# Kernel tuning notes

Measured on AMD Instinct MI355X. Metric: run time of the kernel, lower is better.

Reference implementation:

```python
import jax, jax.numpy as jnp
import numpy as np

N = 50000
E = 800000
NUM_GRAPHS = 128
X_IN, HID, EDGE_DIM = 64, 64, 16


def setup_inputs() -> dict:
    key = jax.random.key(0)
    ks = jax.random.split(key, 9)
    s = 0.05
    inp = {
        'x': jax.random.normal(ks[0], (N, X_IN), jnp.float32),
        'edge_index': jax.random.randint(ks[1], (2, E), 0, N, dtype=jnp.int32),
        'edge_attr': jax.random.normal(ks[2], (E, EDGE_DIM), jnp.float32),
        'batch': jnp.sort(jax.random.randint(ks[3], (N,), 0, NUM_GRAPHS, dtype=jnp.int32)),
        'w_fc1': jax.random.normal(ks[4], (EDGE_DIM, 1), jnp.float32) * s,
        'b_fc1': jnp.zeros((1,), jnp.float32),
    }
    dims = [(X_IN, HID), (HID, HID * 2), (HID * 2, HID)]
    for i, (din, dout) in enumerate(dims):
        k1, k2, k3 = jax.random.split(ks[5 + i], 3)
        inp[f'w1_{i}'] = jax.random.normal(k1, (din, dout), jnp.float32) * s
        inp[f'b1_{i}'] = jnp.zeros((dout,), jnp.float32)
        inp[f'w2_{i}'] = jax.random.normal(k2, (din, dout), jnp.float32) * s
        inp[f'w3_{i}'] = jax.random.normal(k3, (din, dout), jnp.float32) * s
        inp[f'b3_{i}'] = jnp.zeros((dout,), jnp.float32)
    return inp


def leconv(x, src, dst, ew, w1, b1, w2, w3, b3):
    # PyG LEConv: out_i = lin3(x_i) + sum_{j->i} e_ji * (lin1(x_j) - lin2(x_i))
    a = x @ w1 + b1          # lin1 (bias=True)   [N, out]
    b = x @ w2               # lin2 (bias=False)  [N, out]
    msg = ew[:, None] * (a[src] - b[dst])          # [E, out]
    agg = jax.ops.segment_sum(msg, dst, num_segments=N)
    return agg + x @ w3 + b3  # lin3 (bias=True)


def reference(x, edge_index, edge_attr, batch,
              w_fc1, b_fc1,
              w1_0, b1_0, w2_0, w3_0, b3_0,
              w1_1, b1_1, w2_1, w3_1, b3_1,
              w1_2, b1_2, w2_2, w3_2, b3_2):
    src, dst = edge_index[0], edge_index[1]
    ew = (edge_attr @ w_fc1 + b_fc1)[:, 0]         # fc1(edge_attr).squeeze(-1) -> [E]
    h = jax.nn.elu(leconv(x, src, dst, ew, w1_0, b1_0, w2_0, w3_0, b3_0))
    h = jax.nn.elu(leconv(h, src, dst, ew, w1_1, b1_1, w2_1, w3_1, b3_1))
    h = jax.nn.elu(leconv(h, src, dst, ew, w1_2, b1_2, w2_2, w3_2, b3_2))
    # global max pool over nodes of each graph -> [NUM_GRAPHS, HID]
    return jax.ops.segment_max(h, batch, num_segments=NUM_GRAPHS)
```

## Files before the change

### kernel.cpp

```cpp
#include <hip/hip_runtime.h>
#include <math.h>

#define N_NODES 50000
#define N_EDGES 800000
#define NUM_GRAPHS_ 128
#define SCAN_NB 98
#define NPASS 4
#define NODES_PER_PASS 12500
#define HCHUNKS 128
#define EDGES_PER_CHUNK 6250
#define HWORDS 12500
#define TS_BPH 196

typedef unsigned short u16;
typedef unsigned int u32;
typedef __attribute__((ext_vector_type(8))) short bf16x8;
typedef __attribute__((ext_vector_type(4))) float f32x4;

__device__ __forceinline__ float elu_f(float v) {
    return v > 0.f ? v : (__expf(v) - 1.f);
}
__device__ __forceinline__ u16 f2bf(float f) {
    u32 u = __float_as_uint(f);
    u += 0x7FFFu + ((u >> 16) & 1u);
    return (u16)(u >> 16);
}
__device__ __forceinline__ float bf2f(u16 h) {
    return __uint_as_float(((u32)h) << 16);
}
__device__ __forceinline__ void bfpair(u32 v, float& lo, float& hi) {
    lo = __uint_as_float(v << 16);
    hi = __uint_as_float(v & 0xFFFF0000u);
}
__device__ __forceinline__ u32 packbf(float lo, float hi) {
    return (u32)f2bf(lo) | ((u32)f2bf(hi) << 16);
}

__global__ void prep_kernel(const float* __restrict__ edge_attr,
                            const float* __restrict__ w_fc1,
                            const float* __restrict__ b_fc1,
                            const int* __restrict__ edge_index,
                            float* __restrict__ ew,
                            u16* __restrict__ dst16,
                            const float* __restrict__ x, u16* __restrict__ xb,
                            const float* __restrict__ w3_0, const float* __restrict__ w1_0, const float* __restrict__ w2_0,
                            const float* __restrict__ w3_1, const float* __restrict__ w1_1, const float* __restrict__ w2_1,
                            const float* __restrict__ w3_2, const float* __restrict__ w1_2, const float* __restrict__ w2_2,
                            u16* __restrict__ bp0, u16* __restrict__ bp1, u16* __restrict__ bp2) {
    const int b = blockIdx.x;
    if (b < 3125) {
        const int e = b * 256 + threadIdx.x;
        const float4* ea = (const float4*)(edge_attr + (size_t)e * 16);
        const float4* wf = (const float4*)w_fc1;
        float acc = b_fc1[0];
#pragma unroll
        for (int i = 0; i < 4; i++) {
            float4 a = ea[i], w = wf[i];
            acc += a.x * w.x + a.y * w.y + a.z * w.z + a.w * w.w;
        }
        ew[e] = acc;
        dst16[e] = (u16)edge_index[N_EDGES + e];
    } else if (b < 6250) {
        const int g = (b - 3125) * 256 + threadIdx.x;
        float4 v = ((const float4*)x)[g];
        uint2 o;
        o.x = packbf(v.x, v.y);
        o.y = packbf(v.z, v.w);
        ((uint2*)xb)[g] = o;
    } else {
        const int t = (b - 6250) * 256 + threadIdx.x;
        u16 buf[8];
        if (t < 4608) {
            int DOUT, lid;
            const float *w3, *w1, *w2;
            u16* bp;
            if (t < 1536) { DOUT = 64;  lid = t;        w3 = w3_0; w1 = w1_0; w2 = w2_0; bp = bp0; }
            else          { DOUT = 128; lid = t - 1536; w3 = w3_1; w1 = w1_1; w2 = w2_1; bp = bp1; }
            const int NT = DOUT / 16;
            const int lane = lid & 63;
            const int fragid = lid >> 6;
            const int chunk = fragid / NT;
            const int ntile = fragid % NT;
            const int n = ntile * 16 + (lane & 15);
            const int kbase = chunk * 32 + (lane >> 4) * 8;
#pragma unroll
            for (int j = 0; j < 8; j++) {
                int k = kbase + j;
                int region = k / 64;
                int kk = k - region * 64;
                float v = (region == 0) ? w3[kk * DOUT + n]
                        : (region == 1) ? w1[kk * DOUT + n]
                                        : -w2[kk * DOUT + n];
                buf[j] = f2bf(v);
            }
            *(bf16x8*)(bp + ((size_t)lid << 3)) = *(bf16x8*)buf;
        } else if (t < 7680) {
            const int lid = t - 4608;
            const int NT = 12;
            const int lane = lid & 63;
            const int fragid = lid >> 6;
            const int chunk = fragid / NT;
            const int ntile = fragid % NT;
            const int n = ntile * 16 + (lane & 15);
            const int kbase = chunk * 32 + (lane >> 4) * 8;
#pragma unroll
            for (int j = 0; j < 8; j++) {
                int k = kbase + j;
                float v = (n < 64)  ? w3_2[k * 64 + n]
                        : (n < 128) ? -w2_2[k * 64 + (n - 64)]
                                    : w1_2[k * 64 + (n - 128)];
                buf[j] = f2bf(v);
            }
            *(bf16x8*)(bp2 + ((size_t)lid << 3)) = *(bf16x8*)buf;
        }
    }
}

__global__ __launch_bounds__(256) void deg_hist_kernel(const u16* __restrict__ dst16,
                                                       u32* __restrict__ partial) {
    __shared__ u32 bins[HWORDS];
    const int c = blockIdx.x >> 1;
    const int p = blockIdx.x & 1;
    const int t = threadIdx.x;
    for (int i = t; i < HWORDS; i += 256) bins[i] = 0;
    __syncthreads();
    const int base = c * EDGES_PER_CHUNK;
    const int nlo = p * 25000;
    for (int i = t; i < EDGES_PER_CHUNK; i += 256) {
        const int b = (int)dst16[base + i] - nlo;
        if ((unsigned)b < 25000u)
            atomicAdd(&bins[b >> 1], 1u << ((b & 1) * 16));
    }
    __syncthreads();
    u32* outp = partial + (size_t)blockIdx.x * HWORDS;
    for (int i = t; i < HWORDS; i += 256) outp[i] = bins[i];
}

__global__ __launch_bounds__(256) void scan_chunks_kernel(const u32* __restrict__ partial,
                                                          u32* __restrict__ prefpack,
                                                          u32* __restrict__ degpack) {
    __shared__ u32 qsums[4][64];
    const int t = threadIdx.x;
    const int p = (blockIdx.x >= TS_BPH) ? 1 : 0;
    const int wh0 = (blockIdx.x - p * TS_BPH) << 6;
    const int wl = t & 63;
    const int cq = t >> 6;
    const int wh = wh0 + wl;
    const bool ok = wh < HWORDS;

    u32 vals[32];
#pragma unroll
    for (int i = 0; i < 32; i++) {
        const int c = cq * 32 + i;
        vals[i] = ok ? partial[(size_t)((c << 1) + p) * HWORDS + wh] : 0u;
    }
    u32 s = 0;
#pragma unroll
    for (int i = 0; i < 32; i++) s += vals[i];
    qsums[cq][wl] = s;
    __syncthreads();
    u32 run = 0;
#pragma unroll
    for (int j = 0; j < 4; j++)
        if (j < cq) run += qsums[j][wl];

    if (ok) {
        const int g = p * HWORDS + wh;
#pragma unroll
        for (int i = 0; i < 32; i++) {
            const int c = cq * 32 + i;
            prefpack[(size_t)c * 25000 + g] = run;
            run += vals[i];
        }
        if (cq == 3) degpack[g] = run;
    }
}

__global__ __launch_bounds__(256) void scan1_kernel(const u32* __restrict__ degpack,
                                                    int* __restrict__ rowptr,
                                                    int* __restrict__ blk_sums) {
    __shared__ int sh[256];
    const int t = threadIdx.x;
    const int base = blockIdx.x * 512;
    const int i0 = base + 2 * t, i1 = i0 + 1;
    int d0 = 0, d1 = 0;
    if (i0 < N_NODES) {
        u32 v = degpack[i0 >> 1];
        d0 = (int)(v & 0xFFFFu);
        d1 = (int)(v >> 16);
    }
    const int pair = d0 + d1;
    int v = pair;
    sh[t] = v;
    __syncthreads();
#pragma unroll
    for (int off = 1; off < 256; off <<= 1) {
        int add = (t >= off) ? sh[t - off] : 0;
        __syncthreads();
        v += add;
        sh[t] = v;
        __syncthreads();
    }
    const int excl = v - pair;
    if (i0 < N_NODES) rowptr[i0] = excl;
    if (i1 < N_NODES) rowptr[i1] = excl + d0;
    if (t == 255) blk_sums[blockIdx.x] = v;
}

__global__ __launch_bounds__(128) void scan2_kernel(const int* __restrict__ blk_sums,
                                                    int* __restrict__ blk_offs,
                                                    int* __restrict__ rowptr) {
    __shared__ int sh[128];
    const int t = threadIdx.x;
    const int orig = (t < SCAN_NB) ? blk_sums[t] : 0;
    int v = orig;
    sh[t] = v;
    __syncthreads();
#pragma unroll
    for (int off = 1; off < 128; off <<= 1) {
        int add = (t >= off) ? sh[t - off] : 0;
        __syncthreads();
        v += add;
        sh[t] = v;
        __syncthreads();
    }
    if (t < SCAN_NB) blk_offs[t] = v - orig;
    if (t == 127) rowptr[N_NODES] = v;
}

__global__ void scan3_kernel(int* __restrict__ rowptr,
                             const int* __restrict__ blk_offs) {
    int i = blockIdx.x * blockDim.x + threadIdx.x;
    if (i >= N_NODES) return;
    rowptr[i] += blk_offs[i >> 9];
}

__global__ __launch_bounds__(256) void place_kernel(const int* __restrict__ edge_index,
                                                    const float* __restrict__ ew,
                                                    const u16* __restrict__ dst16,
                                                    const int* __restrict__ rowptr,
                                                    const u32* __restrict__ prefpack,
                                                    int2* __restrict__ csr) {
    __shared__ int lcur[NODES_PER_PASS];
    const int pass = blockIdx.x & (NPASS - 1);
    const int c = blockIdx.x >> 2;
    const int lo = pass * NODES_PER_PASS;
    const int t = threadIdx.x;
    for (int i = t; i < NODES_PER_PASS; i += 256) lcur[i] = 0;
    __syncthreads();
    const int base = c * EDGES_PER_CHUNK;
    for (int i = t; i < EDGES_PER_CHUNK; i += 256) {
        const int e = base + i;
        const int d = (int)dst16[e];
        const int dl = d - lo;
        if ((unsigned)dl < (unsigned)NODES_PER_PASS) {
            u32 pw = prefpack[(size_t)c * 25000 + (d >> 1)];
            int pref = (int)((pw >> ((d & 1) * 16)) & 0xFFFFu);
            int lpos = atomicAdd(&lcur[dl], 1);
            int2 ent;
            ent.x = edge_index[e];
            ent.y = __float_as_int(ew[e]);
            csr[rowptr[d] + pref + lpos] = ent;
        }
    }
}

__global__ __launch_bounds__(1024) void fused_l0(
    const u16* __restrict__ xb, const int* __restrict__ rowptr,
    const int2* __restrict__ csr, const u16* __restrict__ Bp0,
    const float* __restrict__ bias1, const float* __restrict__ bias3,
    float* __restrict__ cvec, u16* __restrict__ h1out) {
    __shared__ u16 A[64][200];
    __shared__ float csh[64];
    const int tid = threadIdx.x;
    const int wv = tid >> 6;
    const int lane = tid & 63;
    const int node_base = blockIdx.x * 64;
    const uint2* x2 = (const uint2*)xb;
    const int cg = lane & 15;
    const int eg = lane >> 4;

    for (int k = 0; k < 4; k++) {
        const int row = wv * 4 + k;
        const int node = node_base + row;
        float a0 = 0.f, a1 = 0.f, a2 = 0.f, a3 = 0.f;
        float b0 = 0.f, b1 = 0.f, b2 = 0.f, b3 = 0.f;
        float wsum = 0.f;
        if (node < N_NODES) {
            const int beg = rowptr[node];
            const int end = rowptr[node + 1];
            int p = beg + eg;
            for (; p + 4 < end; p += 8) {
                int2 e0 = csr[p];
                int2 e1 = csr[p + 4];
                float w0 = __int_as_float(e0.y);
                float w1 = __int_as_float(e1.y);
                uint2 v0 = x2[(size_t)e0.x * 16 + cg];
                uint2 v1 = x2[(size_t)e1.x * 16 + cg];
                float f0, f1, f2, f3, g0, g1, g2, g3;
                bfpair(v0.x, f0, f1); bfpair(v0.y, f2, f3);
                bfpair(v1.x, g0, g1); bfpair(v1.y, g2, g3);
                a0 += w0 * f0; a1 += w0 * f1; a2 += w0 * f2; a3 += w0 * f3;
                b0 += w1 * g0; b1 += w1 * g1; b2 += w1 * g2; b3 += w1 * g3;
                wsum += w0 + w1;
            }
            if (p < end) {
                int2 e0 = csr[p];
                float w0 = __int_as_float(e0.y);
                uint2 v0 = x2[(size_t)e0.x * 16 + cg];
                float f0, f1, f2, f3;
                bfpair(v0.x, f0, f1); bfpair(v0.y, f2, f3);
                a0 += w0 * f0; a1 += w0 * f1; a2 += w0 * f2; a3 += w0 * f3;
                wsum += w0;
            }
        }
        a0 += b0; a1 += b1; a2 += b2; a3 += b3;
#pragma unroll
        for (int off = 32; off >= 16; off >>= 1) {
            a0 += __shfl_xor(a0, off);
            a1 += __shfl_xor(a1, off);
            a2 += __shfl_xor(a2, off);
            a3 += __shfl_xor(a3, off);
            wsum += __shfl_xor(wsum, off);
        }
        if (lane < 16) {
            const float cn = wsum;
            uint2 hv = (node < N_NODES) ? x2[(size_t)node * 16 + cg] : (uint2){0u, 0u};
            uint2 so;
            so.x = packbf(a0, a1);
            so.y = packbf(a2, a3);
            *(uint2*)&A[row][cg * 4] = hv;
            *(uint2*)&A[row][64 + cg * 4] = so;
            float h0, h1f, h2f, h3f;
            bfpair(hv.x, h0, h1f); bfpair(hv.y, h2f, h3f);
            uint2 co;
            co.x = packbf(cn * h0, cn * h1f);
            co.y = packbf(cn * h2f, cn * h3f);
            *(uint2*)&A[row][128 + cg * 4] = co;
            if (cg == 0) {
                csh[row] = cn;
                if (node < N_NODES) cvec[node] = cn;
            }
        }
    }
    __syncthreads();

    const int l15 = lane & 15;
    const int q = lane >> 4;
    const int qo = q * 8;
    const int mt = wv >> 2, nt = wv & 3;
    f32x4 acc = {0.f, 0.f, 0.f, 0.f};
#pragma unroll
    for (int chunk = 0; chunk < 6; chunk++) {
        bf16x8 a = *(const bf16x8*)&A[mt * 16 + l15][chunk * 32 + qo];
        bf16x8 b = *(const bf16x8*)(Bp0 + (((size_t)(chunk * 4 + nt) * 64 + lane) << 3));
        acc = __builtin_amdgcn_mfma_f32_16x16x32_bf16(a, b, acc, 0, 0, 0);
    }
    const int col = nt * 16 + l15;
    const float B3 = bias3[col];
    const float B1 = bias1[col];
#pragma unroll
    for (int reg = 0; reg < 4; reg++) {
        const int lrow = mt * 16 + q * 4 + reg;
        const int row = node_base + lrow;
        if (row < N_NODES) {
            const float val = acc[reg] + B3 + csh[lrow] * B1;
            h1out[(size_t)row * 64 + col] = f2bf(elu_f(val));
        }
    }
}

__global__ __launch_bounds__(1024) void fused_l1(
    const u16* __restrict__ h1in, const int* __restrict__ rowptr,
    const int2* __restrict__ csr, const u16* __restrict__ Bp1,
    const u16* __restrict__ Bp2, const float* __restrict__ bias1,
    const float* __restrict__ bias3, u16* __restrict__ zuy) {
    __shared__ u16 A[64][200];
    __shared__ u16 ht[64][136];
    __shared__ float csh[64];
    const int tid = threadIdx.x;
    const int wv = tid >> 6;
    const int lane = tid & 63;
    const int node_base = blockIdx.x * 64;
    const uint2* x2 = (const uint2*)h1in;
    const int cg = lane & 15;
    const int eg = lane >> 4;

    for (int k = 0; k < 4; k++) {
        const int row = wv * 4 + k;
        const int node = node_base + row;
        float a0 = 0.f, a1 = 0.f, a2 = 0.f, a3 = 0.f;
        float b0 = 0.f, b1 = 0.f, b2 = 0.f, b3 = 0.f;
        float wsum = 0.f;
        if (node < N_NODES) {
            const int beg = rowptr[node];
            const int end = rowptr[node + 1];
            int p = beg + eg;
            for (; p + 4 < end; p += 8) {
                int2 e0 = csr[p];
                int2 e1 = csr[p + 4];
                float w0 = __int_as_float(e0.y);
                float w1 = __int_as_float(e1.y);
                uint2 v0 = x2[(size_t)e0.x * 16 + cg];
                uint2 v1 = x2[(size_t)e1.x * 16 + cg];
                float f0, f1, f2, f3, g0, g1, g2, g3;
                bfpair(v0.x, f0, f1); bfpair(v0.y, f2, f3);
                bfpair(v1.x, g0, g1); bfpair(v1.y, g2, g3);
                a0 += w0 * f0; a1 += w0 * f1; a2 += w0 * f2; a3 += w0 * f3;
                b0 += w1 * g0; b1 += w1 * g1; b2 += w1 * g2; b3 += w1 * g3;
                wsum += w0 + w1;
            }
            if (p < end) {
                int2 e0 = csr[p];
                float w0 = __int_as_float(e0.y);
                uint2 v0 = x2[(size_t)e0.x * 16 + cg];
                float f0, f1, f2, f3;
                bfpair(v0.x, f0, f1); bfpair(v0.y, f2, f3);
                a0 += w0 * f0; a1 += w0 * f1; a2 += w0 * f2; a3 += w0 * f3;
                wsum += w0;
            }
        }
        a0 += b0; a1 += b1; a2 += b2; a3 += b3;
#pragma unroll
        for (int off = 32; off >= 16; off >>= 1) {
            a0 += __shfl_xor(a0, off);
            a1 += __shfl_xor(a1, off);
            a2 += __shfl_xor(a2, off);
            a3 += __shfl_xor(a3, off);
            wsum += __shfl_xor(wsum, off);
        }
        if (lane < 16) {
            const float cn = wsum;
            uint2 hv = (node < N_NODES) ? x2[(size_t)node * 16 + cg] : (uint2){0u, 0u};
            uint2 so;
            so.x = packbf(a0, a1);
            so.y = packbf(a2, a3);
            *(uint2*)&A[row][cg * 4] = hv;
            *(uint2*)&A[row][64 + cg * 4] = so;
            float h0, h1f, h2f, h3f;
            bfpair(hv.x, h0, h1f); bfpair(hv.y, h2f, h3f);
            uint2 co;
            co.x = packbf(cn * h0, cn * h1f);
            co.y = packbf(cn * h2f, cn * h3f);
            *(uint2*)&A[row][128 + cg * 4] = co;
            if (cg == 0) csh[row] = cn;
        }
    }
    __syncthreads();

    const int l15 = lane & 15;
    const int q = lane >> 4;
    const int qo = q * 8;

    {
        const int mt = wv >> 2;
        const int nt0 = (wv & 3) * 2;
        f32x4 acc0 = {0.f, 0.f, 0.f, 0.f};
        f32x4 acc1 = {0.f, 0.f, 0.f, 0.f};
#pragma unroll
        for (int chunk = 0; chunk < 6; chunk++) {
            bf16x8 a = *(const bf16x8*)&A[mt * 16 + l15][chunk * 32 + qo];
            bf16x8 bf0 = *(const bf16x8*)(Bp1 + (((size_t)(chunk * 8 + nt0) * 64 + lane) << 3));
            bf16x8 bf1 = *(const bf16x8*)(Bp1 + (((size_t)(chunk * 8 + nt0 + 1) * 64 + lane) << 3));
            acc0 = __builtin_amdgcn_mfma_f32_16x16x32_bf16(a, bf0, acc0, 0, 0, 0);
            acc1 = __builtin_amdgcn_mfma_f32_16x16x32_bf16(a, bf1, acc1, 0, 0, 0);
        }
#pragma unroll
        for (int ni = 0; ni < 2; ni++) {
            const int col = (nt0 + ni) * 16 + l15;
            const float B3 = bias3[col];
            const float B1 = bias1[col];
            const f32x4 av = ni ? acc1 : acc0;
#pragma unroll
            for (int reg = 0; reg < 4; reg++) {
                const int lrow = mt * 16 + q * 4 + reg;
                ht[lrow][col] = f2bf(elu_f(av[reg] + B3 + csh[lrow] * B1));
            }
        }
    }
    __syncthreads();

    {
        const int mt = wv >> 2;
        const int ntb = (wv & 3) * 3;
        f32x4 acc[3] = {};
#pragma unroll
        for (int chunk = 0; chunk < 4; chunk++) {
            bf16x8 a = *(const bf16x8*)&ht[mt * 16 + l15][chunk * 32 + qo];
#pragma unroll
            for (int j = 0; j < 3; j++) {
                bf16x8 b = *(const bf16x8*)(Bp2 + (((size_t)(chunk * 12 + ntb + j) * 64 + lane) << 3));
                acc[j] = __builtin_amdgcn_mfma_f32_16x16x32_bf16(a, b, acc[j], 0, 0, 0);
            }
        }
#pragma unroll
        for (int j = 0; j < 3; j++) {
            const int col = (ntb + j) * 16 + l15;
#pragma unroll
            for (int reg = 0; reg < 4; reg++) {
                const int row = node_base + mt * 16 + q * 4 + reg;
                if (row < N_NODES)
                    zuy[(size_t)row * 192 + col] = f2bf(acc[j][reg]);
            }
        }
    }
}

__global__ __launch_bounds__(256) void gather2_kernel(
    const u16* __restrict__ zuy, const int* __restrict__ rowptr,
    const int2* __restrict__ csr, const float* __restrict__ c,
    const float* __restrict__ bias1, const float* __restrict__ bias3,
    u16* __restrict__ h3) {
    constexpr int CG = 16, EG = 4;
    const int gid = blockIdx.x * 256 + threadIdx.x;
    const int node = gid >> 6;
    if (node >= N_NODES) return;
    const int lane = threadIdx.x & 63;
    const int cg = lane & (CG - 1);
    const int eg = lane >> 4;
    const int beg = rowptr[node];
    const int end = rowptr[node + 1];

    float a0 = 0.f, a1 = 0.f, a2 = 0.f, a3 = 0.f;
    float b0 = 0.f, b1 = 0.f, b2 = 0.f, b3 = 0.f;

    int p = beg + eg;
    for (; p + EG < end; p += 2 * EG) {
        int2 e0 = csr[p];
        int2 e1 = csr[p + EG];
        float w0 = __int_as_float(e0.y);
        float w1 = __int_as_float(e1.y);
        uint2 v0 = ((const uint2*)(zuy + (size_t)e0.x * 192 + 128))[cg];
        uint2 v1 = ((const uint2*)(zuy + (size_t)e1.x * 192 + 128))[cg];
        float f0, f1, f2, f3, g0, g1, g2, g3;
        bfpair(v0.x, f0, f1); bfpair(v0.y, f2, f3);
        bfpair(v1.x, g0, g1); bfpair(v1.y, g2, g3);
        a0 += w0 * f0; a1 += w0 * f1; a2 += w0 * f2; a3 += w0 * f3;
        b0 += w1 * g0; b1 += w1 * g1; b2 += w1 * g2; b3 += w1 * g3;
    }
    if (p < end) {
        int2 e0 = csr[p];
        float w0 = __int_as_float(e0.y);
        uint2 v0 = ((const uint2*)(zuy + (size_t)e0.x * 192 + 128))[cg];
        float f0, f1, f2, f3;
        bfpair(v0.x, f0, f1); bfpair(v0.y, f2, f3);
        a0 += w0 * f0; a1 += w0 * f1; a2 += w0 * f2; a3 += w0 * f3;
    }
    a0 += b0; a1 += b1; a2 += b2; a3 += b3;

#pragma unroll
    for (int off = 32; off >= CG; off >>= 1) {
        a0 += __shfl_xor(a0, off);
        a1 += __shfl_xor(a1, off);
        a2 += __shfl_xor(a2, off);
        a3 += __shfl_xor(a3, off);
    }

    if (lane < CG) {
        const float cn = c[node];
        const u16* zr = zuy + (size_t)node * 192;
        uint2 zv = ((const uint2*)zr)[cg];
        uint2 uv = ((const uint2*)(zr + 64))[cg];
        float z0, z1, z2, z3, u0, u1, u2, u3;
        bfpair(zv.x, z0, z1); bfpair(zv.y, z2, z3);
        bfpair(uv.x, u0, u1); bfpair(uv.y, u2, u3);
        const float4 b3v = *(const float4*)(bias3 + cg * 4);
        const float4 b1v = *(const float4*)(bias1 + cg * 4);
        float o0 = elu_f(z0 + cn * u0 + a0 + b3v.x + cn * b1v.x);
        float o1 = elu_f(z1 + cn * u1 + a1 + b3v.y + cn * b1v.y);
        float o2 = elu_f(z2 + cn * u2 + a2 + b3v.z + cn * b1v.z);
        float o3 = elu_f(z3 + cn * u3 + a3 + b3v.w + cn * b1v.w);
        uint2 o;
        o.x = packbf(o0, o1);
        o.y = packbf(o2, o3);
        ((uint2*)h3)[(size_t)node * CG + cg] = o;
    }
}

__global__ void pool_kernel(const u16* __restrict__ h,
                            const int* __restrict__ batch,
                            float* __restrict__ out) {
    const int g = blockIdx.x;
    const int tid = threadIdx.x;
    int lo = 0, hi = N_NODES;
    while (lo < hi) { int mid = (lo + hi) >> 1; if (batch[mid] < g) lo = mid + 1; else hi = mid; }
    const int beg = lo;
    lo = beg; hi = N_NODES;
    while (lo < hi) { int mid = (lo + hi) >> 1; if (batch[mid] < g + 1) lo = mid + 1; else hi = mid; }
    const int end = lo;

    __shared__ float red[256];
    const int col = tid & 63;
    const int rg = tid >> 6;
    float m = -3.0e38f;
    for (int r = beg + rg; r < end; r += 4) m = fmaxf(m, bf2f(h[(size_t)r * 64 + col]));
    red[tid] = m;
    __syncthreads();
    if (tid < 64) {
        m = fmaxf(fmaxf(red[tid], red[tid + 64]), fmaxf(red[tid + 128], red[tid + 192]));
        out[g * 64 + tid] = m;
    }
}

extern "C" void kernel_launch(void* const* d_in, const int* in_sizes, int n_in,
                              void* d_out, int out_size, void* d_ws, size_t ws_size,
                              hipStream_t stream) {
    const float* x = (const float*)d_in[0];
    const int* ei = (const int*)d_in[1];
    const float* ea = (const float*)d_in[2];
    const int* batch = (const int*)d_in[3];
    const float* wfc = (const float*)d_in[4];
    const float* bfc = (const float*)d_in[5];
    const float* w1_0 = (const float*)d_in[6];
    const float* b1_0 = (const float*)d_in[7];
    const float* w2_0 = (const float*)d_in[8];
    const float* w3_0 = (const float*)d_in[9];
    const float* b3_0 = (const float*)d_in[10];
    const float* w1_1 = (const float*)d_in[11];
    const float* b1_1 = (const float*)d_in[12];
    const float* w2_1 = (const float*)d_in[13];
    const float* w3_1 = (const float*)d_in[14];
    const float* b3_1 = (const float*)d_in[15];
    const float* w1_2 = (const float*)d_in[16];
    const float* b1_2 = (const float*)d_in[17];
    const float* w2_2 = (const float*)d_in[18];
    const float* w3_2 = (const float*)d_in[19];
    const float* b3_2 = (const float*)d_in[20];
    float* out = (float*)d_out;

    char* ws = (char*)d_ws;
    float* ew      = (float*)(ws);
    float* c       = (float*)(ws + 3200000);
    int*   rowptr  = (int*)  (ws + 3800000);
    int2*  csr     = (int2*) (ws + 4000128);
    u16*   xb      = (u16*)  (ws + 10400128);
    u32*   partial = (u32*)  (ws + 16800128);
    u16*   dst16   = (u16*)  (ws + 29600128);
    u32*   degpack = (u32*)  (ws + 31600128);
    u16*   h1      = (u16*)  (ws + 42400128);
    u16*   zuy     = (u16*)  (ws + 48800128);
    u16*   bp0     = (u16*)  (ws + 68000128);
    u16*   bp1     = (u16*)  (ws + 68024704);
    u16*   bp2     = (u16*)  (ws + 68073856);
    int* blk_sums  = (int*)  (ws + 68123008);
    int* blk_offs  = (int*)  (ws + 68123520);
    u32* prefpack = (u32*)zuy;
    u16* h3 = xb;

    prep_kernel<<<6280, 256, 0, stream>>>(ea, wfc, bfc, ei, ew, dst16, x, xb,
                                          w3_0, w1_0, w2_0, w3_1, w1_1, w2_1,
                                          w3_2, w1_2, w2_2, bp0, bp1, bp2);
    deg_hist_kernel<<<HCHUNKS * 2, 256, 0, stream>>>(dst16, partial);
    scan_chunks_kernel<<<TS_BPH * 2, 256, 0, stream>>>(partial, prefpack, degpack);
    scan1_kernel<<<SCAN_NB, 256, 0, stream>>>(degpack, rowptr, blk_sums);
    scan2_kernel<<<1, 128, 0, stream>>>(blk_sums, blk_offs, rowptr);
    scan3_kernel<<<(N_NODES + 255) / 256, 256, 0, stream>>>(rowptr, blk_offs);
    place_kernel<<<HCHUNKS * NPASS, 256, 0, stream>>>(ei, ew, dst16, rowptr, prefpack, csr);

    const int RB = (N_NODES + 63) / 64;
    const int GBLK = (N_NODES * 64 + 255) / 256;

    fused_l0<<<RB, 1024, 0, stream>>>(xb, rowptr, csr, bp0, b1_0, b3_0, c, h1);

    fused_l1<<<RB, 1024, 0, stream>>>(h1, rowptr, csr, bp1, bp2, b1_1, b3_1, zuy);

    gather2_kernel<<<GBLK, 256, 0, stream>>>(zuy, rowptr, csr, c, b1_2, b3_2, h3);

    pool_kernel<<<NUM_GRAPHS_, 256, 0, stream>>>(h3, batch, out);
}
```

Measured before the change: 318.5 us.

## Unroll CSR gathers four-deep and split zuy into contiguous zu and y buffers

Adds a shared gather helper that keeps four independent edge loads in flight per lane with separate accumulators, replacing the two-deep loops in fused_l0, fused_l1 and gather2. It also splits the interleaved 192-wide zuy output into a 128-wide zu buffer and a dense 64-wide y buffer, so the layer-2 gather reads compact 128-byte rows instead of strided slices. The aim is more memory-level parallelism and better cache-line use in the latency-bound gathers, at the cost of more registers and an extra branch on the store path.

```diff
diff --git a/kernel.cpp b/kernel.cpp
--- a/kernel.cpp
+++ b/kernel.cpp
@@ -34,6 +34,53 @@
 }
 __device__ __forceinline__ u32 packbf(float lo, float hi) {
     return (u32)f2bf(lo) | ((u32)f2bf(hi) << 16);
+}
+
+__device__ __forceinline__ void gather_rows4(
+    const int2* __restrict__ csr, const uint2* __restrict__ x2,
+    int beg, int end, int eg, int cg, int rowstride2,
+    float& A0, float& A1, float& A2, float& A3, float& WS) {
+    float a0 = 0.f, a1 = 0.f, a2 = 0.f, a3 = 0.f, ws0 = 0.f;
+    float b0 = 0.f, b1 = 0.f, b2 = 0.f, b3 = 0.f, ws1 = 0.f;
+    float c0 = 0.f, c1 = 0.f, c2 = 0.f, c3 = 0.f, ws2 = 0.f;
+    float d0 = 0.f, d1 = 0.f, d2 = 0.f, d3 = 0.f, ws3 = 0.f;
+    int p = beg + eg;
+    for (; p + 12 < end; p += 16) {
+        int2 e0 = csr[p];
+        int2 e1 = csr[p + 4];
+        int2 e2 = csr[p + 8];
+        int2 e3 = csr[p + 12];
+        uint2 v0 = x2[(size_t)e0.x * rowstride2 + cg];
+        uint2 v1 = x2[(size_t)e1.x * rowstride2 + cg];
+        uint2 v2 = x2[(size_t)e2.x * rowstride2 + cg];
+        uint2 v3 = x2[(size_t)e3.x * rowstride2 + cg];
+        float w0 = __int_as_float(e0.y);
+        float w1 = __int_as_float(e1.y);
+        float w2 = __int_as_float(e2.y);
+        float w3 = __int_as_float(e3.y);
+        float f0, f1, f2, f3;
+        bfpair(v0.x, f0, f1); bfpair(v0.y, f2, f3);
+        a0 += w0 * f0; a1 += w0 * f1; a2 += w0 * f2; a3 += w0 * f3; ws0 += w0;
+        bfpair(v1.x, f0, f1); bfpair(v1.y, f2, f3);
+        b0 += w1 * f0; b1 += w1 * f1; b2 += w1 * f2; b3 += w1 * f3; ws1 += w1;
+        bfpair(v2.x, f0, f1); bfpair(v2.y, f2, f3);
+        c0 += w2 * f0; c1 += w2 * f1; c2 += w2 * f2; c3 += w2 * f3; ws2 += w2;
+        bfpair(v3.x, f0, f1); bfpair(v3.y, f2, f3);
+        d0 += w3 * f0; d1 += w3 * f1; d2 += w3 * f2; d3 += w3 * f3; ws3 += w3;
+    }
+    for (; p < end; p += 4) {
+        int2 e0 = csr[p];
+        uint2 v0 = x2[(size_t)e0.x * rowstride2 + cg];
+        float w0 = __int_as_float(e0.y);
+        float f0, f1, f2, f3;
+        bfpair(v0.x, f0, f1); bfpair(v0.y, f2, f3);
+        a0 += w0 * f0; a1 += w0 * f1; a2 += w0 * f2; a3 += w0 * f3; ws0 += w0;
+    }
+    A0 = (a0 + b0) + (c0 + d0);
+    A1 = (a1 + b1) + (c1 + d1);
+    A2 = (a2 + b2) + (c2 + d2);
+    A3 = (a3 + b3) + (c3 + d3);
+    WS = (ws0 + ws1) + (ws2 + ws3);
 }
 
 __global__ void prep_kernel(const float* __restrict__ edge_attr,
@@ -283,38 +330,10 @@
     for (int k = 0; k < 4; k++) {
         const int row = wv * 4 + k;
         const int node = node_base + row;
-        float a0 = 0.f, a1 = 0.f, a2 = 0.f, a3 = 0.f;
-        float b0 = 0.f, b1 = 0.f, b2 = 0.f, b3 = 0.f;
-        float wsum = 0.f;
-        if (node < N_NODES) {
-            const int beg = rowptr[node];
-            const int end = rowptr[node + 1];
-            int p = beg + eg;
-            for (; p + 4 < end; p += 8) {
-                int2 e0 = csr[p];
-                int2 e1 = csr[p + 4];
-                float w0 = __int_as_float(e0.y);
-                float w1 = __int_as_float(e1.y);
-                uint2 v0 = x2[(size_t)e0.x * 16 + cg];
-                uint2 v1 = x2[(size_t)e1.x * 16 + cg];
-                float f0, f1, f2, f3, g0, g1, g2, g3;
-                bfpair(v0.x, f0, f1); bfpair(v0.y, f2, f3);
-                bfpair(v1.x, g0, g1); bfpair(v1.y, g2, g3);
-                a0 += w0 * f0; a1 += w0 * f1; a2 += w0 * f2; a3 += w0 * f3;
-                b0 += w1 * g0; b1 += w1 * g1; b2 += w1 * g2; b3 += w1 * g3;
-                wsum += w0 + w1;
-            }
-            if (p < end) {
-                int2 e0 = csr[p];
-                float w0 = __int_as_float(e0.y);
-                uint2 v0 = x2[(size_t)e0.x * 16 + cg];
-                float f0, f1, f2, f3;
-                bfpair(v0.x, f0, f1); bfpair(v0.y, f2, f3);
-                a0 += w0 * f0; a1 += w0 * f1; a2 += w0 * f2; a3 += w0 * f3;
-                wsum += w0;
-            }
-        }
-        a0 += b0; a1 += b1; a2 += b2; a3 += b3;
+        float a0 = 0.f, a1 = 0.f, a2 = 0.f, a3 = 0.f, wsum = 0.f;
+        if (node < N_NODES)
+            gather_rows4(csr, x2, rowptr[node], rowptr[node + 1], eg, cg, 16,
+                         a0, a1, a2, a3, wsum);
 #pragma unroll
         for (int off = 32; off >= 16; off >>= 1) {
             a0 += __shfl_xor(a0, off);
@@ -374,7 +393,8 @@
     const u16* __restrict__ h1in, const int* __restrict__ rowptr,
     const int2* __restrict__ csr, const u16* __restrict__ Bp1,
     const u16* __restrict__ Bp2, const float* __restrict__ bias1,
-    const float* __restrict__ bias3, u16* __restrict__ zuy) {
+    const float* __restrict__ bias3, u16* __restrict__ zu,
+    u16* __restrict__ yb) {
     __shared__ u16 A[64][200];
     __shared__ u16 ht[64][136];
     __shared__ float csh[64];
@@ -389,38 +409,10 @@
     for (int k = 0; k < 4; k++) {
         const int row = wv * 4 + k;
         const int node = node_base + row;
-        float a0 = 0.f, a1 = 0.f, a2 = 0.f, a3 = 0.f;
-        float b0 = 0.f, b1 = 0.f, b2 = 0.f, b3 = 0.f;
-        float wsum = 0.f;
-        if (node < N_NODES) {
-            const int beg = rowptr[node];
-            const int end = rowptr[node + 1];
-            int p = beg + eg;
-            for (; p + 4 < end; p += 8) {
-                int2 e0 = csr[p];
-                int2 e1 = csr[p + 4];
-                float w0 = __int_as_float(e0.y);
-                float w1 = __int_as_float(e1.y);
-                uint2 v0 = x2[(size_t)e0.x * 16 + cg];
-                uint2 v1 = x2[(size_t)e1.x * 16 + cg];
-                float f0, f1, f2, f3, g0, g1, g2, g3;
-                bfpair(v0.x, f0, f1); bfpair(v0.y, f2, f3);
-                bfpair(v1.x, g0, g1); bfpair(v1.y, g2, g3);
-                a0 += w0 * f0; a1 += w0 * f1; a2 += w0 * f2; a3 += w0 * f3;
-                b0 += w1 * g0; b1 += w1 * g1; b2 += w1 * g2; b3 += w1 * g3;
-                wsum += w0 + w1;
-            }
-            if (p < end) {
-                int2 e0 = csr[p];
-                float w0 = __int_as_float(e0.y);
-                uint2 v0 = x2[(size_t)e0.x * 16 + cg];
-                float f0, f1, f2, f3;
-                bfpair(v0.x, f0, f1); bfpair(v0.y, f2, f3);
-                a0 += w0 * f0; a1 += w0 * f1; a2 += w0 * f2; a3 += w0 * f3;
-                wsum += w0;
-            }
-        }
-        a0 += b0; a1 += b1; a2 += b2; a3 += b3;
+        float a0 = 0.f, a1 = 0.f, a2 = 0.f, a3 = 0.f, wsum = 0.f;
+        if (node < N_NODES)
+            gather_rows4(csr, x2, rowptr[node], rowptr[node + 1], eg, cg, 16,
+                         a0, a1, a2, a3, wsum);
 #pragma unroll
         for (int off = 32; off >= 16; off >>= 1) {
             a0 += __shfl_xor(a0, off);
@@ -499,54 +491,32 @@
 #pragma unroll
             for (int reg = 0; reg < 4; reg++) {
                 const int row = node_base + mt * 16 + q * 4 + reg;
-                if (row < N_NODES)
-                    zuy[(size_t)row * 192 + col] = f2bf(acc[j][reg]);
+                if (row < N_NODES) {
+                    const u16 v = f2bf(acc[j][reg]);
+                    if (col < 128) zu[(size_t)row * 128 + col] = v;
+                    else           yb[(size_t)row * 64 + (col - 128)] = v;
+                }
             }
         }
     }
 }
 
 __global__ __launch_bounds__(256) void gather2_kernel(
-    const u16* __restrict__ zuy, const int* __restrict__ rowptr,
-    const int2* __restrict__ csr, const float* __restrict__ c,
-    const float* __restrict__ bias1, const float* __restrict__ bias3,
-    u16* __restrict__ h3) {
-    constexpr int CG = 16, EG = 4;
+    const u16* __restrict__ zu, const u16* __restrict__ yb,
+    const int* __restrict__ rowptr, const int2* __restrict__ csr,
+    const float* __restrict__ c, const float* __restrict__ bias1,
+    const float* __restrict__ bias3, u16* __restrict__ h3) {
+    constexpr int CG = 16;
     const int gid = blockIdx.x * 256 + threadIdx.x;
     const int node = gid >> 6;
     if (node >= N_NODES) return;
     const int lane = threadIdx.x & 63;
     const int cg = lane & (CG - 1);
     const int eg = lane >> 4;
-    const int beg = rowptr[node];
-    const int end = rowptr[node + 1];
-
-    float a0 = 0.f, a1 = 0.f, a2 = 0.f, a3 = 0.f;
-    float b0 = 0.f, b1 = 0.f, b2 = 0.f, b3 = 0.f;
-
-    int p = beg + eg;
-    for (; p + EG < end; p += 2 * EG) {
-        int2 e0 = csr[p];
-        int2 e1 = csr[p + EG];
-        float w0 = __int_as_float(e0.y);
-        float w1 = __int_as_float(e1.y);
-        uint2 v0 = ((const uint2*)(zuy + (size_t)e0.x * 192 + 128))[cg];
-        uint2 v1 = ((const uint2*)(zuy + (size_t)e1.x * 192 + 128))[cg];
-        float f0, f1, f2, f3, g0, g1, g2, g3;
-        bfpair(v0.x, f0, f1); bfpair(v0.y, f2, f3);
-        bfpair(v1.x, g0, g1); bfpair(v1.y, g2, g3);
-        a0 += w0 * f0; a1 += w0 * f1; a2 += w0 * f2; a3 += w0 * f3;
-        b0 += w1 * g0; b1 += w1 * g1; b2 += w1 * g2; b3 += w1 * g3;
-    }
-    if (p < end) {
-        int2 e0 = csr[p];
-        float w0 = __int_as_float(e0.y);
-        uint2 v0 = ((const uint2*)(zuy + (size_t)e0.x * 192 + 128))[cg];
-        float f0, f1, f2, f3;
-        bfpair(v0.x, f0, f1); bfpair(v0.y, f2, f3);
-        a0 += w0 * f0; a1 += w0 * f1; a2 += w0 * f2; a3 += w0 * f3;
-    }
-    a0 += b0; a1 += b1; a2 += b2; a3 += b3;
+
+    float a0, a1, a2, a3, wdummy;
+    gather_rows4(csr, (const uint2*)yb, rowptr[node], rowptr[node + 1], eg, cg, 16,
+                 a0, a1, a2, a3, wdummy);
 
 #pragma unroll
     for (int off = 32; off >= CG; off >>= 1) {
@@ -558,7 +528,7 @@
 
     if (lane < CG) {
         const float cn = c[node];
-        const u16* zr = zuy + (size_t)node * 192;
+        const u16* zr = zu + (size_t)node * 128;
         uint2 zv = ((const uint2*)zr)[cg];
         uint2 uv = ((const uint2*)(zr + 64))[cg];
         float z0, z1, z2, z3, u0, u1, u2, u3;
@@ -638,13 +608,14 @@
     u16*   dst16   = (u16*)  (ws + 29600128);
     u32*   degpack = (u32*)  (ws + 31600128);
     u16*   h1      = (u16*)  (ws + 42400128);
-    u16*   zuy     = (u16*)  (ws + 48800128);
+    u16*   zu      = (u16*)  (ws + 48800128);
+    u16*   yb      = (u16*)  (ws + 61600128);
     u16*   bp0     = (u16*)  (ws + 68000128);
     u16*   bp1     = (u16*)  (ws + 68024704);
     u16*   bp2     = (u16*)  (ws + 68073856);
     int* blk_sums  = (int*)  (ws + 68123008);
     int* blk_offs  = (int*)  (ws + 68123520);
-    u32* prefpack = (u32*)zuy;
+    u32* prefpack = (u32*)zu;
     u16* h3 = xb;
 
     prep_kernel<<<6280, 256, 0, stream>>>(ea, wfc, bfc, ei, ew, dst16, x, xb,
@@ -662,9 +633,9 @@
 
     fused_l0<<<RB, 1024, 0, stream>>>(xb, rowptr, csr, bp0, b1_0, b3_0, c, h1);
 
-    fused_l1<<<RB, 1024, 0, stream>>>(h1, rowptr, csr, bp1, bp2, b1_1, b3_1, zuy);
-
-    gather2_kernel<<<GBLK, 256, 0, stream>>>(zuy, rowptr, csr, c, b1_2, b3_2, h3);
+    fused_l1<<<RB, 1024, 0, stream>>>(h1, rowptr, csr, bp1, bp2, b1_1, b3_1, zu, yb);
+
+    gather2_kernel<<<GBLK, 256, 0, stream>>>(zu, yb, rowptr, csr, c, b1_2, b3_2, h3);
 
     pool_kernel<<<NUM_GRAPHS_, 256, 0, stream>>>(h3, batch, out);
 }
```

New measurement: 328.4 us. 3.1% more time.
